# Performance work log

Measured on AMD Instinct MI355X. Metric: run time of the kernel, lower is better.

The kernel has to match this reference:

```python
import jax, jax.numpy as jnp
import numpy as np

HIDDEN = 2048
NUM_V = 16
NUM_K = 8
HK = 128
HV = 128
KCONV = 4
KEY_DIM = NUM_K * HK      # 1024
VALUE_DIM = NUM_V * HV    # 2048
CONV_DIM = 2 * KEY_DIM + VALUE_DIM  # 4096
R = NUM_V // NUM_K        # 2
L2_EPS = 1e-6
NORM_EPS = 1e-6


def setup_inputs() -> dict:
    key = jax.random.key(0)
    ks = jax.random.split(key, 8)
    s = 0.02
    return {
        "hidden_states": jax.random.normal(ks[0], (1, 1024, HIDDEN), jnp.float32),
        "w_qkvz": jax.random.normal(ks[1], (2 * KEY_DIM + 2 * VALUE_DIM, HIDDEN), jnp.float32) * s,
        "w_ba": jax.random.normal(ks[2], (2 * NUM_V, HIDDEN), jnp.float32) * s,
        "conv_w": jax.random.normal(ks[3], (CONV_DIM, KCONV), jnp.float32) * s,
        "dt_bias": jnp.ones((NUM_V,), jnp.float32),
        "A_log": jnp.log(jax.random.uniform(ks[4], (NUM_V,), jnp.float32, 1e-3, 16.0)),
        "norm_weight": jnp.ones((HV,), jnp.float32),
        "w_out": jax.random.normal(ks[5], (HIDDEN, VALUE_DIM), jnp.float32) * s,
    }


def reference(hidden_states, w_qkvz, w_ba, conv_w, dt_bias, A_log, norm_weight, w_out):
    B, T, _ = hidden_states.shape
    # --- input projections ---
    qkvz = hidden_states @ w_qkvz.T                     # [B,T,2K+2V]
    ba = hidden_states @ w_ba.T                         # [B,T,2*Hv]
    # fix_query_key_value_ordering: group by k-head, layout [hk, hk, r*hv, r*hv]
    qkvz = qkvz.reshape(B, T, NUM_K, 2 * HK + 2 * R * HV)
    q, k, v, z = jnp.split(qkvz, [HK, 2 * HK, 2 * HK + R * HV], axis=3)
    v = v.reshape(B, T, NUM_V, HV)
    z = z.reshape(B, T, NUM_V, HV)
    ba = ba.reshape(B, T, NUM_K, 2 * R)
    b = ba[..., :R].reshape(B, T, NUM_V)
    a = ba[..., R:].reshape(B, T, NUM_V)
    # --- depthwise causal conv1d + silu over concatenated q,k,v ---
    mixed = jnp.concatenate(
        [q.reshape(B, T, KEY_DIM), k.reshape(B, T, KEY_DIM), v.reshape(B, T, VALUE_DIM)], axis=-1
    )
    xc = mixed.transpose(0, 2, 1)                       # [B,C,T]
    yc = jax.lax.conv_general_dilated(
        xc, conv_w[:, None, :], (1,), [(KCONV - 1, 0)],
        feature_group_count=CONV_DIM, dimension_numbers=("NCH", "OIH", "NCH"),
    )
    yc = jax.nn.silu(yc).transpose(0, 2, 1)             # [B,T,C]
    q, k, v = jnp.split(yc, [KEY_DIM, 2 * KEY_DIM], axis=-1)
    q = q.reshape(B, T, NUM_K, HK)
    k = k.reshape(B, T, NUM_K, HK)
    v = v.reshape(B, T, NUM_V, HV)
    # --- gates ---
    beta = jax.nn.sigmoid(b)                            # [B,T,Hv]
    g = -jnp.exp(A_log) * jax.nn.softplus(a + dt_bias)  # [B,T,Hv] (log decay, <=0)
    # GQA expansion of q,k to value heads
    q = jnp.repeat(q, R, axis=2)                        # [B,T,Hv,hk]
    k = jnp.repeat(k, R, axis=2)
    # l2 norm on q,k (use_qk_l2norm_in_kernel=True)
    q = q * jax.lax.rsqrt(jnp.sum(q * q, -1, keepdims=True) + L2_EPS)
    k = k * jax.lax.rsqrt(jnp.sum(k * k, -1, keepdims=True) + L2_EPS)
    scale = HK ** -0.5
    # --- gated delta rule recurrence ---
    def step(S, xs):
        qt, kt, vt, gt, bt = xs                          # per-timestep slices
        S = S * jnp.exp(gt)[..., None, None]             # decay state [B,Hv,hk,hv]
        kv = jnp.einsum("bhk,bhkv->bhv", kt, S)          # readout at k_t
        delta = (vt - kv) * bt[..., None]                # beta-gated delta
        S = S + jnp.einsum("bhk,bhv->bhkv", kt, delta)
        o = jnp.einsum("bhk,bhkv->bhv", qt * scale, S)
        return S, o

    S0 = jnp.zeros((B, NUM_V, HK, HV), hidden_states.dtype)
    xs = (
        q.transpose(1, 0, 2, 3), k.transpose(1, 0, 2, 3), v.transpose(1, 0, 2, 3),
        g.transpose(1, 0, 2), beta.transpose(1, 0, 2),
    )
    _, o = jax.lax.scan(step, S0, xs)                   # o: [T,B,Hv,hv]
    o = o.transpose(1, 0, 2, 3)                         # [B,T,Hv,hv]
    # --- gated RMSNorm (gate applied before normalization, Mamba2/Qwen3Next style) ---
    xf = o.astype(jnp.float32) * jax.nn.silu(z.astype(jnp.float32))
    var = jnp.mean(xf * xf, -1, keepdims=True)
    xn = xf * jax.lax.rsqrt(var + NORM_EPS) * norm_weight
    # --- output projection ---
    return xn.reshape(B, T, VALUE_DIM) @ w_out.T
```

## Files before the change

kernel.cpp:

```cpp
#include <hip/hip_runtime.h>
#include <math.h>

#define T_LEN   1024
#define HIDDEN  2048
#define QKVZ_N  6144
#define VAL_DIM 2048

typedef _Float16 half8 __attribute__((ext_vector_type(8)));
typedef _Float16 half4 __attribute__((ext_vector_type(4)));
typedef _Float16 half2t __attribute__((ext_vector_type(2)));
typedef float floatx4 __attribute__((ext_vector_type(4)));

__device__ __forceinline__ float sigmoidf_(float x) { return 1.f / (1.f + expf(-x)); }

__device__ __forceinline__ void gl_lds16(const _Float16* g, _Float16* l) {
    __builtin_amdgcn_global_load_lds(
        (const __attribute__((address_space(1))) void*)g,
        (__attribute__((address_space(3))) void*)l, 16, 0, 0);
}

__global__ __launch_bounds__(256) void cvt3(const float* __restrict__ s0, _Float16* __restrict__ d0, int n0,
                                            const float* __restrict__ s1, _Float16* __restrict__ d1, int n1,
                                            const float* __restrict__ s2, _Float16* __restrict__ d2, int n2) {
    int i = blockIdx.x * 256 + threadIdx.x;
    const float* s;
    _Float16* d;
    if (i < n0) { s = s0; d = d0; }
    else if (i < n0 + n1) { s = s1; d = d1; i -= n0; }
    else if (i < n0 + n1 + n2) { s = s2; d = d2; i -= n0 + n1; }
    else return;
    const float4 v = ((const float4*)s)[i];
    half4 h;
    h[0] = (_Float16)v.x; h[1] = (_Float16)v.y;
    h[2] = (_Float16)v.z; h[3] = (_Float16)v.w;
    *(half4*)&d[i * 4] = h;
}

template <typename OutT>
__global__ __launch_bounds__(256, 2) void gemm_h16(const _Float16* __restrict__ A,
                                                   const _Float16* __restrict__ W,
                                                   OutT* __restrict__ C,
                                                   int MB, int NB, int K) {
    const int N = NB * 128;
    const int l = blockIdx.x;
    const int x = l & 7;
    const int tt = l >> 3;
    const int mb = tt % MB;
    const int nb = x + 8 * (tt / MB);
    const int m0 = mb * 64, n0 = nb * 128;

    const int t = threadIdx.x;
    const int wave = t >> 6;
    const int lane = t & 63;
    const int wr = (wave >> 1) * 32;
    const int wc = (wave & 1) * 64;
    const int l15 = lane & 15;
    const int quad = lane >> 4;
    const int srow = lane >> 3;
    const int slot = lane & 7;

    __shared__ __align__(16) _Float16 Ah[2][4096];
    __shared__ __align__(16) _Float16 Bh[2][8192];

    floatx4 acc[2][4];
#pragma unroll
    for (int i = 0; i < 2; ++i)
#pragma unroll
        for (int j = 0; j < 4; ++j) acc[i][j] = 0;

    auto stage = [&](int buf, int k0) {
#pragma unroll
        for (int g = 0; g < 2; ++g) {
            const int r = wave * 16 + g * 8 + srow;
            const int kc = slot ^ (r & 7);
            gl_lds16(A + (size_t)(m0 + r) * K + k0 + kc * 8,
                     &Ah[buf][(wave * 128 + g * 64) * 8]);
        }
#pragma unroll
        for (int g = 0; g < 4; ++g) {
            const int r = wave * 32 + g * 8 + srow;
            const int kc = slot ^ (r & 7);
            gl_lds16(W + (size_t)(n0 + r) * K + k0 + kc * 8,
                     &Bh[buf][(wave * 256 + g * 64) * 8]);
        }
    };

    const int NIT = K >> 6;
    stage(0, 0);
    __syncthreads();
    int cur = 0;
    for (int it = 0; it < NIT; ++it) {
        if (it + 1 < NIT) stage(cur ^ 1, (it + 1) * 64);
        half8 af[2][2], bf[4][2];
#pragma unroll
        for (int mt = 0; mt < 2; ++mt)
#pragma unroll
            for (int ks = 0; ks < 2; ++ks) {
                const int m = wr + mt * 16 + l15;
                const int kq = ks * 4 + quad;
                af[mt][ks] = *(const half8*)&Ah[cur][(m * 8 + (kq ^ (m & 7))) * 8];
            }
#pragma unroll
        for (int nt = 0; nt < 4; ++nt)
#pragma unroll
            for (int ks = 0; ks < 2; ++ks) {
                const int n = wc + nt * 16 + l15;
                const int kq = ks * 4 + quad;
                bf[nt][ks] = *(const half8*)&Bh[cur][(n * 8 + (kq ^ (n & 7))) * 8];
            }
#pragma unroll
        for (int mt = 0; mt < 2; ++mt)
#pragma unroll
            for (int nt = 0; nt < 4; ++nt)
#pragma unroll
                for (int ks = 0; ks < 2; ++ks)
                    acc[mt][nt] = __builtin_amdgcn_mfma_f32_16x16x32_f16(
                        af[mt][ks], bf[nt][ks], acc[mt][nt], 0, 0, 0);
        if (it + 1 < NIT) {
            __syncthreads();
            cur ^= 1;
        }
    }
#pragma unroll
    for (int mt = 0; mt < 2; ++mt)
#pragma unroll
        for (int nt = 0; nt < 4; ++nt) {
            const int c = n0 + wc + nt * 16 + l15;
#pragma unroll
            for (int reg = 0; reg < 4; ++reg) {
                const int r = m0 + wr + mt * 16 + quad * 4 + reg;
                C[(size_t)r * N + c] = (OutT)acc[mt][nt][reg];
            }
        }
}

__global__ __launch_bounds__(256) void gemm_ba_gates(const float* __restrict__ A,
                                                     const float* __restrict__ W,
                                                     const float* __restrict__ dt_bias,
                                                     const float* __restrict__ A_log,
                                                     float* __restrict__ lgd,
                                                     float* __restrict__ bet) {
    const int m = blockIdx.x;
    const int tid = threadIdx.x;
    const int kl = tid & 31;
    const int ng = tid >> 5;
    const float* Arow = A + (size_t)m * 2048;
    __shared__ float sba[32];

    float4 a4[16];
#pragma unroll
    for (int j = 0; j < 16; ++j)
        a4[j] = *(const float4*)(Arow + j * 128 + kl * 4);

#pragma unroll
    for (int nn = 0; nn < 4; ++nn) {
        const int n = nn * 8 + ng;
        const float* Wrow = W + (size_t)n * 2048;
        float acc = 0.f;
#pragma unroll
        for (int j = 0; j < 16; ++j) {
            const float4 w4 = *(const float4*)(Wrow + j * 128 + kl * 4);
            acc = fmaf(a4[j].x, w4.x, acc);
            acc = fmaf(a4[j].y, w4.y, acc);
            acc = fmaf(a4[j].z, w4.z, acc);
            acc = fmaf(a4[j].w, w4.w, acc);
        }
        acc += __shfl_xor(acc, 1, 64);
        acc += __shfl_xor(acc, 2, 64);
        acc += __shfl_xor(acc, 4, 64);
        acc += __shfl_xor(acc, 8, 64);
        acc += __shfl_xor(acc, 16, 64);
        if (kl == 0) sba[n] = acc;
    }
    __syncthreads();
    if (tid < 16) {
        const int vh = tid, kh = vh >> 1, r = vh & 1;
        const float b = sba[kh * 4 + r];
        const float a = sba[kh * 4 + 2 + r];
        bet[m * 16 + vh] = 1.f / (1.f + expf(-b));
        const float xx = a + dt_bias[vh];
        const float sp = (xx > 0.f) ? (xx + log1pf(expf(-xx))) : log1pf(expf(xx));
        lgd[m * 16 + vh] = -expf(A_log[vh]) * sp;
    }
}

__global__ __launch_bounds__(512) void conv_silu_l2(const _Float16* __restrict__ qkvz,
                                                    const float* __restrict__ conv_w,
                                                    _Float16* __restrict__ qc,
                                                    _Float16* __restrict__ kc,
                                                    _Float16* __restrict__ vc) {
    const int t = blockIdx.x;
    const int c = threadIdx.x * 8;
    int col;
    _Float16* dst;
    bool isqk;
    float extra = 1.f;
    if (c < 1024) {
        col = ((c >> 7) * 768) + (c & 127);
        dst = qc + t * 1024 + c;
        isqk = true;
        extra = 0.08838834764831845f;
    } else if (c < 2048) {
        const int cc = c - 1024;
        col = ((cc >> 7) * 768) + 128 + (cc & 127);
        dst = kc + t * 1024 + cc;
        isqk = true;
    } else {
        const int cc = c - 2048;
        col = ((cc >> 8) * 768) + 256 + (cc & 255);
        dst = vc + (size_t)t * 2048 + cc;
        isqk = false;
    }
    const size_t gb = (size_t)t * QKVZ_N + col;
    const half8 x3 = *(const half8*)(qkvz + gb);
    half8 x2, x1, x0;
    if (t >= 1) x2 = *(const half8*)(qkvz + gb - QKVZ_N);
    if (t >= 2) x1 = *(const half8*)(qkvz + gb - 2 * (size_t)QKVZ_N);
    if (t >= 3) x0 = *(const half8*)(qkvz + gb - 3 * (size_t)QKVZ_N);

    float y[8];
    float ss = 0.f;
#pragma unroll
    for (int u = 0; u < 8; ++u) {
        const float4 wv = *(const float4*)(conv_w + (c + u) * 4);
        float acc = (float)x3[u] * wv.w;
        if (t >= 1) acc = fmaf((float)x2[u], wv.z, acc);
        if (t >= 2) acc = fmaf((float)x1[u], wv.y, acc);
        if (t >= 3) acc = fmaf((float)x0[u], wv.x, acc);
        acc = acc * (1.f / (1.f + expf(-acc)));
        y[u] = acc;
        ss = fmaf(acc, acc, ss);
    }
    half8 ov;
    if (isqk) {
        ss += __shfl_xor(ss, 1, 64);
        ss += __shfl_xor(ss, 2, 64);
        ss += __shfl_xor(ss, 4, 64);
        ss += __shfl_xor(ss, 8, 64);
        const float r = rsqrtf(ss + 1e-6f) * extra;
#pragma unroll
        for (int u = 0; u < 8; ++u) ov[u] = (_Float16)(y[u] * r);
    } else {
#pragma unroll
        for (int u = 0; u < 8; ++u) ov[u] = (_Float16)y[u];
    }
    *(half8*)dst = ov;
}

__global__ __launch_bounds__(256) void chunk_prep(
    const _Float16* __restrict__ qch, const _Float16* __restrict__ kch,
    const _Float16* __restrict__ vch, const float* __restrict__ lgd,
    const float* __restrict__ bet, _Float16* __restrict__ CH,
    float* __restrict__ gamC) {
    const int blk = blockIdx.x;
    const int c = blk >> 4, h = blk & 15, kh = h >> 1;
    const int c0 = c * 64;
    const int tid = threadIdx.x, lane = tid & 63, wave = tid >> 6;
    const int l15 = lane & 15, quad = lane >> 4;

    __shared__ __align__(16) _Float16 Ksh[8192];
    __shared__ __align__(16) _Float16 Qsh[8192];
    __shared__ float Amat[64 * 65];
    __shared__ float Gs[64], Bets[64], Gam[64];

    {
        const int t = tid >> 2, kc0 = (tid & 3) * 4;
        const size_t gb = (size_t)(c0 + t) * 1024 + kh * 128;
#pragma unroll
        for (int i = 0; i < 4; ++i) {
            const int kc = kc0 + i;
            half8 kv = *(const half8*)(kch + gb + kc * 8);
            half8 qv = *(const half8*)(qch + gb + kc * 8);
            const int chl = t * 16 + (kc ^ (t & 15));
            *(half8*)&Ksh[chl * 8] = kv;
            *(half8*)&Qsh[chl * 8] = qv;
        }
    }
    if (tid < 64) {
        float g = lgd[(size_t)(c0 + tid) * 16 + h];
#pragma unroll
        for (int off = 1; off < 64; off <<= 1) {
            float y = __shfl_up(g, off, 64);
            if (tid >= off) g += y;
        }
        Gs[tid] = g;
        Gam[tid] = expf(g);
        Bets[tid] = bet[(size_t)(c0 + tid) * 16 + h];
    }
    __syncthreads();

    _Float16* CHb = CH + (size_t)(c * 16 + h) * 36864;
    _Float16* Ug = CHb;
    _Float16* Wtg = CHb + 8192;
    _Float16* Khg = CHb + 16384;
    _Float16* Qgg = CHb + 24576;
    _Float16* Lg = CHb + 32768;

    {
        floatx4 accKK[4], accQK[4];
#pragma unroll
        for (int tt = 0; tt < 4; ++tt) { accKK[tt] = 0; accQK[tt] = 0; }
        half8 bfK[4];
#pragma unroll
        for (int ks = 0; ks < 4; ++ks) {
            const int i = wave * 16 + l15;
            const int kc = ks * 4 + quad;
            bfK[ks] = *(const half8*)&Ksh[(i * 16 + (kc ^ (i & 15))) * 8];
        }
#pragma unroll
        for (int tt = 0; tt < 4; ++tt) {
            const int t = tt * 16 + l15;
#pragma unroll
            for (int ks = 0; ks < 4; ++ks) {
                const int kc = ks * 4 + quad;
                const int chl = (t * 16 + (kc ^ (t & 15))) * 8;
                half8 afK = *(const half8*)&Ksh[chl];
                half8 afQ = *(const half8*)&Qsh[chl];
                accKK[tt] = __builtin_amdgcn_mfma_f32_16x16x32_f16(afK, bfK[ks], accKK[tt], 0, 0, 0);
                accQK[tt] = __builtin_amdgcn_mfma_f32_16x16x32_f16(afQ, bfK[ks], accQK[tt], 0, 0, 0);
            }
        }
        const int ii = wave * 16 + l15;
        const float Gi = Gs[ii];
#pragma unroll
        for (int tt = 0; tt < 4; ++tt)
#pragma unroll
            for (int r = 0; r < 4; ++r) {
                const int t = tt * 16 + quad * 4 + r;
                const float Gt = Gs[t];
                const float ratio = (ii <= t) ? expf(Gt - Gi) : 0.f;
                if (ii < t) Amat[t * 65 + ii] = Bets[t] * ratio * accKK[tt][r];
                Lg[t * 64 + ii] = (_Float16)((ii <= t) ? ratio * accQK[tt][r] : 0.f);
            }
    }
    __syncthreads();

    {
        const int j = tid;
        float x[64];
        if (j < 128) {
#pragma unroll
            for (int t = 0; t < 64; ++t)
                x[t] = Bets[t] * (float)vch[(size_t)(c0 + t) * 2048 + h * 128 + j];
        } else {
            const int k = j - 128;
#pragma unroll
            for (int t = 0; t < 64; ++t) {
                const int chl = t * 16 + ((k >> 3) ^ (t & 15));
                x[t] = Bets[t] * Gam[t] * (float)Ksh[chl * 8 + (k & 7)];
            }
        }
#pragma unroll
        for (int t = 1; t < 64; ++t) {
            float acc = 0.f;
#pragma unroll
            for (int i = 0; i < t; ++i) acc = fmaf(Amat[t * 65 + i], x[i], acc);
            x[t] -= acc;
        }
        if (j < 128) {
#pragma unroll
            for (int t = 0; t < 64; t += 4) {
                half4 w4;
                w4[0] = (_Float16)x[t]; w4[1] = (_Float16)x[t + 1];
                w4[2] = (_Float16)x[t + 2]; w4[3] = (_Float16)x[t + 3];
                *(half4*)&Wtg[j * 64 + t] = w4;
            }
        } else {
            const int k = j - 128;
#pragma unroll
            for (int t = 0; t < 64; ++t) Ug[t * 128 + k] = (_Float16)x[t];
        }
    }

    {
        const float g63 = Gs[63];
        const int k = tid >> 1, cb = (tid & 1) * 32;
#pragma unroll
        for (int cc = 0; cc < 32; cc += 4) {
            half4 o4;
#pragma unroll
            for (int u = 0; u < 4; ++u) {
                const int ci = cb + cc + u;
                const int chl = ci * 16 + ((k >> 3) ^ (ci & 15));
                o4[u] = (_Float16)(expf(g63 - Gs[ci]) * (float)Ksh[chl * 8 + (k & 7)]);
            }
            *(half4*)&Khg[k * 64 + cb + cc] = o4;
        }
        const int cq = tid >> 2, kb = (tid & 3) * 4;
        const float gam = Gam[cq];
#pragma unroll
        for (int kc = 0; kc < 4; ++kc) {
            const int kcc = kb + kc;
            half8 q8 = *(const half8*)&Qsh[(cq * 16 + (kcc ^ (cq & 15))) * 8];
            half8 s8;
#pragma unroll
            for (int u = 0; u < 8; ++u) s8[u] = (_Float16)(gam * (float)q8[u]);
            *(half8*)&Qgg[cq * 128 + kcc * 8] = s8;
        }
        if (tid == 0) gamC[c * 16 + h] = Gam[63];
    }
}

__global__ __launch_bounds__(256) void chunk_scan(const _Float16* __restrict__ CH,
                                                  const float* __restrict__ gamC,
                                                  float* __restrict__ o) {
    const int h = blockIdx.x >> 1, vs = blockIdx.x & 1;
    const int tid = threadIdx.x, lane = tid & 63, wave = tid >> 6;
    const int l15 = lane & 15, quad = lane >> 4;
    const int vrow = wave * 16 + l15;

    __shared__ __align__(16) _Float16 Sh[8192];
    __shared__ __align__(16) _Float16 Dt[4096];
    __shared__ __align__(16) _Float16 LUg[8704];
    __shared__ __align__(16) _Float16 LWt[4608];
    __shared__ __align__(16) _Float16 LKh[9216];
    __shared__ __align__(16) _Float16 LQg[8704];
    __shared__ __align__(16) _Float16 LLg[4608];

    floatx4 Sacc[8];
#pragma unroll
    for (int kt = 0; kt < 8; ++kt) Sacc[kt] = 0;
    for (int i = tid; i < 1024; i += 256) *(int4*)&Sh[i * 8] = make_int4(0, 0, 0, 0);
    __syncthreads();

    for (int c = 0; c < 16; ++c) {
        const _Float16* CHb = CH + (size_t)(c * 16 + h) * 36864;
        {
            const int4* src = (const int4*)CHb;
#pragma unroll
            for (int i = 0; i < 4; ++i) {
                const int idx = tid + i * 256;
                *(int4*)&LUg[((idx >> 4) * 17 + (idx & 15)) * 8] = src[idx];
            }
        }
        {
            const int4* src = (const int4*)(CHb + 8192 + vs * 4096);
#pragma unroll
            for (int i = 0; i < 2; ++i) {
                const int idx = tid + i * 256;
                *(int4*)&LWt[((idx >> 3) * 9 + (idx & 7)) * 8] = src[idx];
            }
        }
        {
            const int4* src = (const int4*)(CHb + 16384);
#pragma unroll
            for (int i = 0; i < 4; ++i) {
                const int idx = tid + i * 256;
                *(int4*)&LKh[((idx >> 3) * 9 + (idx & 7)) * 8] = src[idx];
            }
        }
        {
            const int4* src = (const int4*)(CHb + 24576);
#pragma unroll
            for (int i = 0; i < 4; ++i) {
                const int idx = tid + i * 256;
                *(int4*)&LQg[((idx >> 4) * 17 + (idx & 15)) * 8] = src[idx];
            }
        }
        {
            const int4* src = (const int4*)(CHb + 32768);
#pragma unroll
            for (int i = 0; i < 2; ++i) {
                const int idx = tid + i * 256;
                *(int4*)&LLg[((idx >> 3) * 9 + (idx & 7)) * 8] = src[idx];
            }
        }
        __syncthreads();

        half8 bs[4];
#pragma unroll
        for (int ks = 0; ks < 4; ++ks) {
            const int kc = ks * 4 + quad;
            bs[ks] = *(const half8*)&Sh[(vrow * 16 + (kc ^ (vrow & 15))) * 8];
        }
#pragma unroll
        for (int ct = 0; ct < 4; ++ct) {
            floatx4 xa = {0.f, 0.f, 0.f, 0.f};
#pragma unroll
            for (int ks = 0; ks < 4; ++ks) {
                half8 af = *(const half8*)&LUg[((ct * 16 + l15) * 17 + ks * 4 + quad) * 8];
                xa = __builtin_amdgcn_mfma_f32_16x16x32_f16(af, bs[ks], xa, 0, 0, 0);
            }
            half4 w4 = *(const half4*)&LWt[(vrow * 9 + ct * 2 + (quad >> 1)) * 8 + (quad & 1) * 4];
            half4 d4;
#pragma unroll
            for (int r = 0; r < 4; ++r) d4[r] = (_Float16)((float)w4[r] - xa[r]);
            const int cc = ct * 2 + (quad >> 1);
            *(half4*)&Dt[(vrow * 8 + (cc ^ (vrow & 7))) * 8 + (quad & 1) * 4] = d4;
        }
        half8 bd[2];
#pragma unroll
        for (int cs = 0; cs < 2; ++cs) {
            const int cc = cs * 4 + quad;
            bd[cs] = *(const half8*)&Dt[(vrow * 8 + (cc ^ (vrow & 7))) * 8];
        }
#pragma unroll
        for (int ct = 0; ct < 4; ++ct) {
            floatx4 oa = {0.f, 0.f, 0.f, 0.f};
#pragma unroll
            for (int ks = 0; ks < 4; ++ks) {
                half8 af = *(const half8*)&LQg[((ct * 16 + l15) * 17 + ks * 4 + quad) * 8];
                oa = __builtin_amdgcn_mfma_f32_16x16x32_f16(af, bs[ks], oa, 0, 0, 0);
            }
#pragma unroll
            for (int cs = 0; cs < 2; ++cs) {
                half8 af = *(const half8*)&LLg[((ct * 16 + l15) * 9 + cs * 4 + quad) * 8];
                oa = __builtin_amdgcn_mfma_f32_16x16x32_f16(af, bd[cs], oa, 0, 0, 0);
            }
            const int tg = c * 64 + ct * 16 + quad * 4;
            const int col = h * 128 + vs * 64 + vrow;
#pragma unroll
            for (int r = 0; r < 4; ++r) o[(size_t)(tg + r) * 2048 + col] = oa[r];
        }
        const float gC = gamC[c * 16 + h];
#pragma unroll
        for (int kt = 0; kt < 8; ++kt) {
#pragma unroll
            for (int r = 0; r < 4; ++r) Sacc[kt][r] *= gC;
#pragma unroll
            for (int cs = 0; cs < 2; ++cs) {
                half8 af = *(const half8*)&LKh[((kt * 16 + l15) * 9 + cs * 4 + quad) * 8];
                Sacc[kt] = __builtin_amdgcn_mfma_f32_16x16x32_f16(af, bd[cs], Sacc[kt], 0, 0, 0);
            }
        }
#pragma unroll
        for (int kt = 0; kt < 8; ++kt) {
            const int kc = kt * 2 + (quad >> 1);
            half4 s4;
#pragma unroll
            for (int r = 0; r < 4; ++r) s4[r] = (_Float16)Sacc[kt][r];
            *(half4*)&Sh[(vrow * 16 + (kc ^ (vrow & 15))) * 8 + (quad & 1) * 4] = s4;
        }
        __syncthreads();
    }
}

__global__ __launch_bounds__(64) void gated_norm(const float* __restrict__ o,
                                                 const _Float16* __restrict__ qkvz,
                                                 const float* __restrict__ nw,
                                                 _Float16* __restrict__ xn) {
    const int b = blockIdx.x;
    const int t = b >> 4;
    const int vh = b & 15;
    const int kh = vh >> 1;
    const int r = vh & 1;
    const float* op = o + (size_t)t * 2048 + vh * 128;
    const _Float16* zp = qkvz + (size_t)t * QKVZ_N + kh * 768 + 512 + r * 128;
    const int j = threadIdx.x * 2;
    const float2 ov = *(const float2*)(op + j);
    const half2t zv = *(const half2t*)(zp + j);
    const float z0 = (float)zv[0], z1 = (float)zv[1];
    const float f0 = ov.x * z0 / (1.f + expf(-z0));
    const float f1 = ov.y * z1 / (1.f + expf(-z1));
    float ss = f0 * f0 + f1 * f1;
#pragma unroll
    for (int m = 1; m < 64; m <<= 1) ss += __shfl_xor(ss, m, 64);
    const float rs = rsqrtf(ss * (1.f / 128.f) + 1e-6f);
    _Float16* xp = xn + (size_t)t * 2048 + vh * 128;
    half2t y;
    y[0] = (_Float16)(f0 * rs * nw[j]);
    y[1] = (_Float16)(f1 * rs * nw[j + 1]);
    *(half2t*)(xp + j) = y;
}

extern "C" void kernel_launch(void* const* d_in, const int* in_sizes, int n_in,
                              void* d_out, int out_size, void* d_ws, size_t ws_size,
                              hipStream_t stream) {
    const float* hidden  = (const float*)d_in[0];
    const float* w_qkvz  = (const float*)d_in[1];
    const float* w_ba    = (const float*)d_in[2];
    const float* conv_w  = (const float*)d_in[3];
    const float* dt_bias = (const float*)d_in[4];
    const float* A_log   = (const float*)d_in[5];
    const float* norm_w  = (const float*)d_in[6];
    const float* w_out   = (const float*)d_in[7];
    float* out = (float*)d_out;

    char* w = (char*)d_ws;
    _Float16*  qkvz_h = (_Float16*)(w);
    _Float16*  qch    = (_Float16*)(w + 12713984);
    _Float16*  kch    = (_Float16*)(w + 14811136);
    _Float16*  vch    = (_Float16*)(w + 16908288);
    float*     lgd    = (float*)(w + 21102592);
    float*     bet    = (float*)(w + 21168128);
    float*     gamC   = (float*)(w + 21233664);
    float*     o      = (float*)(w + 21237760);
    _Float16*  hid_h  = (_Float16*)(w + 21237760);
    _Float16*  wqk_h  = (_Float16*)(w + 29626368);
    _Float16*  CH     = (_Float16*)(w + 29626368);
    _Float16*  xn_h   = (_Float16*)(w + 29626368 + 18874368);
    _Float16*  wout_h = (_Float16*)(w + 54792192);

    const int n0 = HIDDEN * T_LEN / 4;
    const int n1 = QKVZ_N * HIDDEN / 4;
    const int n2 = VAL_DIM * HIDDEN / 4;
    cvt3<<<(n0 + n1 + n2 + 255) / 256, 256, 0, stream>>>(hidden, hid_h, n0,
                                                         w_qkvz, wqk_h, n1,
                                                         w_out, wout_h, n2);

    gemm_h16<_Float16><<<16 * 48, 256, 0, stream>>>(hid_h, wqk_h, qkvz_h, 16, 48, HIDDEN);
    gemm_ba_gates<<<T_LEN, 256, 0, stream>>>(hidden, w_ba, dt_bias, A_log, lgd, bet);
    conv_silu_l2<<<T_LEN, 512, 0, stream>>>(qkvz_h, conv_w, qch, kch, vch);
    chunk_prep<<<256, 256, 0, stream>>>(qch, kch, vch, lgd, bet, CH, gamC);
    chunk_scan<<<32, 256, 0, stream>>>(CH, gamC, o);
    gated_norm<<<T_LEN * 16, 64, 0, stream>>>(o, qkvz_h, norm_w, xn_h);
    gemm_h16<float><<<16 * 16, 256, 0, stream>>>(xn_h, wout_h, out, 16, 16, HIDDEN);
}
```

Baseline: 298.9 us.

## Split chunk scan into 16-column value slices with register-prefetched operands

```diff
diff --git a/kernel.cpp b/kernel.cpp
--- a/kernel.cpp
+++ b/kernel.cpp
@@ -401,137 +401,109 @@
     }
 }
 
+struct ScanOps {
+    half8 aU[4];
+    half8 aQ[4];
+    half8 aL[2];
+    half8 aK[2][2];
+    half4 wv;
+    float gC;
+};
+
 __global__ __launch_bounds__(256) void chunk_scan(const _Float16* __restrict__ CH,
                                                   const float* __restrict__ gamC,
                                                   float* __restrict__ o) {
-    const int h = blockIdx.x >> 1, vs = blockIdx.x & 1;
+    const int h = blockIdx.x & 15;
+    const int vsl = blockIdx.x >> 4;
     const int tid = threadIdx.x, lane = tid & 63, wave = tid >> 6;
     const int l15 = lane & 15, quad = lane >> 4;
-    const int vrow = wave * 16 + l15;
-
-    __shared__ __align__(16) _Float16 Sh[8192];
-    __shared__ __align__(16) _Float16 Dt[4096];
-    __shared__ __align__(16) _Float16 LUg[8704];
-    __shared__ __align__(16) _Float16 LWt[4608];
-    __shared__ __align__(16) _Float16 LKh[9216];
-    __shared__ __align__(16) _Float16 LQg[8704];
-    __shared__ __align__(16) _Float16 LLg[4608];
-
-    floatx4 Sacc[8];
-#pragma unroll
-    for (int kt = 0; kt < 8; ++kt) Sacc[kt] = 0;
-    for (int i = tid; i < 1024; i += 256) *(int4*)&Sh[i * 8] = make_int4(0, 0, 0, 0);
+    const int tw = wave * 16;
+    const int kw = wave * 32;
+    const int sKey = l15 << 1;
+    const int dKey = (l15 << 1) & 14;
+
+    __shared__ __align__(16) _Float16 Ssh[16 * 128];
+    __shared__ __align__(16) _Float16 Dsh[16 * 64];
+
+    *(half8*)&Ssh[tid * 8] = half8{0, 0, 0, 0, 0, 0, 0, 0};
+    floatx4 Sacc[2];
+    Sacc[0] = 0; Sacc[1] = 0;
     __syncthreads();
 
-    for (int c = 0; c < 16; ++c) {
+    auto loadOps = [&](ScanOps& S, int c) {
         const _Float16* CHb = CH + (size_t)(c * 16 + h) * 36864;
-        {
-            const int4* src = (const int4*)CHb;
-#pragma unroll
-            for (int i = 0; i < 4; ++i) {
-                const int idx = tid + i * 256;
-                *(int4*)&LUg[((idx >> 4) * 17 + (idx & 15)) * 8] = src[idx];
-            }
-        }
-        {
-            const int4* src = (const int4*)(CHb + 8192 + vs * 4096);
-#pragma unroll
-            for (int i = 0; i < 2; ++i) {
-                const int idx = tid + i * 256;
-                *(int4*)&LWt[((idx >> 3) * 9 + (idx & 7)) * 8] = src[idx];
-            }
-        }
-        {
-            const int4* src = (const int4*)(CHb + 16384);
-#pragma unroll
-            for (int i = 0; i < 4; ++i) {
-                const int idx = tid + i * 256;
-                *(int4*)&LKh[((idx >> 3) * 9 + (idx & 7)) * 8] = src[idx];
-            }
-        }
-        {
-            const int4* src = (const int4*)(CHb + 24576);
-#pragma unroll
-            for (int i = 0; i < 4; ++i) {
-                const int idx = tid + i * 256;
-                *(int4*)&LQg[((idx >> 4) * 17 + (idx & 15)) * 8] = src[idx];
-            }
-        }
-        {
-            const int4* src = (const int4*)(CHb + 32768);
-#pragma unroll
-            for (int i = 0; i < 2; ++i) {
-                const int idx = tid + i * 256;
-                *(int4*)&LLg[((idx >> 3) * 9 + (idx & 7)) * 8] = src[idx];
-            }
-        }
+#pragma unroll
+        for (int ks = 0; ks < 4; ++ks) {
+            S.aU[ks] = *(const half8*)(CHb + (tw + l15) * 128 + ks * 32 + quad * 8);
+            S.aQ[ks] = *(const half8*)(CHb + 24576 + (tw + l15) * 128 + ks * 32 + quad * 8);
+        }
+#pragma unroll
+        for (int cs = 0; cs < 2; ++cs) {
+            S.aL[cs] = *(const half8*)(CHb + 32768 + (tw + l15) * 64 + cs * 32 + quad * 8);
+#pragma unroll
+            for (int kt = 0; kt < 2; ++kt)
+                S.aK[kt][cs] = *(const half8*)(CHb + 16384 + (kw + kt * 16 + l15) * 64 + cs * 32 + quad * 8);
+        }
+        S.wv = *(const half4*)(CHb + 8192 + (vsl * 16 + l15) * 64 + tw + quad * 4);
+        S.gC = gamC[c * 16 + h];
+    };
+
+    auto chunkBody = [&](const ScanOps& S, int c) {
+        half8 bs[4];
+#pragma unroll
+        for (int ks = 0; ks < 4; ++ks)
+            bs[ks] = *(const half8*)&Ssh[(l15 * 32 + ((ks * 8 + quad * 2) ^ sKey)) * 4];
+        floatx4 xa = {0.f, 0.f, 0.f, 0.f};
+#pragma unroll
+        for (int ks = 0; ks < 4; ++ks)
+            xa = __builtin_amdgcn_mfma_f32_16x16x32_f16(S.aU[ks], bs[ks], xa, 0, 0, 0);
+        half4 d4;
+#pragma unroll
+        for (int r = 0; r < 4; ++r) d4[r] = (_Float16)((float)S.wv[r] - xa[r]);
+        *(half4*)&Dsh[(l15 * 16 + ((wave * 4 + quad) ^ dKey)) * 4] = d4;
         __syncthreads();
 
-        half8 bs[4];
-#pragma unroll
-        for (int ks = 0; ks < 4; ++ks) {
-            const int kc = ks * 4 + quad;
-            bs[ks] = *(const half8*)&Sh[(vrow * 16 + (kc ^ (vrow & 15))) * 8];
-        }
-#pragma unroll
-        for (int ct = 0; ct < 4; ++ct) {
-            floatx4 xa = {0.f, 0.f, 0.f, 0.f};
-#pragma unroll
-            for (int ks = 0; ks < 4; ++ks) {
-                half8 af = *(const half8*)&LUg[((ct * 16 + l15) * 17 + ks * 4 + quad) * 8];
-                xa = __builtin_amdgcn_mfma_f32_16x16x32_f16(af, bs[ks], xa, 0, 0, 0);
-            }
-            half4 w4 = *(const half4*)&LWt[(vrow * 9 + ct * 2 + (quad >> 1)) * 8 + (quad & 1) * 4];
-            half4 d4;
-#pragma unroll
-            for (int r = 0; r < 4; ++r) d4[r] = (_Float16)((float)w4[r] - xa[r]);
-            const int cc = ct * 2 + (quad >> 1);
-            *(half4*)&Dt[(vrow * 8 + (cc ^ (vrow & 7))) * 8 + (quad & 1) * 4] = d4;
-        }
         half8 bd[2];
 #pragma unroll
-        for (int cs = 0; cs < 2; ++cs) {
-            const int cc = cs * 4 + quad;
-            bd[cs] = *(const half8*)&Dt[(vrow * 8 + (cc ^ (vrow & 7))) * 8];
-        }
-#pragma unroll
-        for (int ct = 0; ct < 4; ++ct) {
-            floatx4 oa = {0.f, 0.f, 0.f, 0.f};
-#pragma unroll
-            for (int ks = 0; ks < 4; ++ks) {
-                half8 af = *(const half8*)&LQg[((ct * 16 + l15) * 17 + ks * 4 + quad) * 8];
-                oa = __builtin_amdgcn_mfma_f32_16x16x32_f16(af, bs[ks], oa, 0, 0, 0);
-            }
-#pragma unroll
-            for (int cs = 0; cs < 2; ++cs) {
-                half8 af = *(const half8*)&LLg[((ct * 16 + l15) * 9 + cs * 4 + quad) * 8];
-                oa = __builtin_amdgcn_mfma_f32_16x16x32_f16(af, bd[cs], oa, 0, 0, 0);
-            }
-            const int tg = c * 64 + ct * 16 + quad * 4;
-            const int col = h * 128 + vs * 64 + vrow;
-#pragma unroll
-            for (int r = 0; r < 4; ++r) o[(size_t)(tg + r) * 2048 + col] = oa[r];
-        }
-        const float gC = gamC[c * 16 + h];
-#pragma unroll
-        for (int kt = 0; kt < 8; ++kt) {
-#pragma unroll
-            for (int r = 0; r < 4; ++r) Sacc[kt][r] *= gC;
-#pragma unroll
-            for (int cs = 0; cs < 2; ++cs) {
-                half8 af = *(const half8*)&LKh[((kt * 16 + l15) * 9 + cs * 4 + quad) * 8];
-                Sacc[kt] = __builtin_amdgcn_mfma_f32_16x16x32_f16(af, bd[cs], Sacc[kt], 0, 0, 0);
-            }
-        }
-#pragma unroll
-        for (int kt = 0; kt < 8; ++kt) {
-            const int kc = kt * 2 + (quad >> 1);
+        for (int cs = 0; cs < 2; ++cs)
+            bd[cs] = *(const half8*)&Dsh[(l15 * 16 + ((cs * 8 + quad * 2) ^ dKey)) * 4];
+        floatx4 oacc = {0.f, 0.f, 0.f, 0.f};
+#pragma unroll
+        for (int ks = 0; ks < 4; ++ks)
+            oacc = __builtin_amdgcn_mfma_f32_16x16x32_f16(S.aQ[ks], bs[ks], oacc, 0, 0, 0);
+#pragma unroll
+        for (int cs = 0; cs < 2; ++cs)
+            oacc = __builtin_amdgcn_mfma_f32_16x16x32_f16(S.aL[cs], bd[cs], oacc, 0, 0, 0);
+#pragma unroll
+        for (int kt = 0; kt < 2; ++kt) {
+#pragma unroll
+            for (int r = 0; r < 4; ++r) Sacc[kt][r] *= S.gC;
+#pragma unroll
+            for (int cs = 0; cs < 2; ++cs)
+                Sacc[kt] = __builtin_amdgcn_mfma_f32_16x16x32_f16(S.aK[kt][cs], bd[cs], Sacc[kt], 0, 0, 0);
+        }
+        const int col = h * 128 + vsl * 16 + l15;
+#pragma unroll
+        for (int r = 0; r < 4; ++r)
+            o[(size_t)(c * 64 + tw + quad * 4 + r) * 2048 + col] = oacc[r];
+#pragma unroll
+        for (int kt = 0; kt < 2; ++kt) {
             half4 s4;
 #pragma unroll
             for (int r = 0; r < 4; ++r) s4[r] = (_Float16)Sacc[kt][r];
-            *(half4*)&Sh[(vrow * 16 + (kc ^ (vrow & 15))) * 8 + (quad & 1) * 4] = s4;
+            *(half4*)&Ssh[(l15 * 32 + ((wave * 8 + kt * 4 + quad) ^ sKey)) * 4] = s4;
         }
         __syncthreads();
+    };
+
+    ScanOps A_, B_;
+    loadOps(A_, 0);
+#pragma unroll 1
+    for (int cc = 0; cc < 16; cc += 2) {
+        loadOps(B_, cc + 1);
+        chunkBody(A_, cc);
+        if (cc + 2 < 16) loadOps(A_, cc + 2);
+        chunkBody(B_, cc + 1);
     }
 }
 
@@ -602,7 +574,7 @@
     gemm_ba_gates<<<T_LEN, 256, 0, stream>>>(hidden, w_ba, dt_bias, A_log, lgd, bet);
     conv_silu_l2<<<T_LEN, 512, 0, stream>>>(qkvz_h, conv_w, qch, kch, vch);
     chunk_prep<<<256, 256, 0, stream>>>(qch, kch, vch, lgd, bet, CH, gamC);
-    chunk_scan<<<32, 256, 0, stream>>>(CH, gamC, o);
+    chunk_scan<<<128, 256, 0, stream>>>(CH, gamC, o);
     gated_norm<<<T_LEN * 16, 64, 0, stream>>>(o, qkvz_h, norm_w, xn_h);
     gemm_h16<float><<<16 * 16, 256, 0, stream>>>(xn_h, wout_h, out, 16, 16, HIDDEN);
 }
```

Result: faster. 286.8 us (-4.0%).
